# Kernel tuning notes

Measured on AMD Instinct MI355X. Metric: run time of the kernel, lower is better.

## Reference

```python
import jax, jax.numpy as jnp
import numpy as np

V, BLK, L, H, C, FF = 50257, 2048, 6, 8, 512, 2048
D = C // H  # head_dim = 64

def setup_inputs() -> dict:
    key = jax.random.key(0)
    ks = jax.random.split(key, 16)
    s = 0.02
    proj_std = 0.02 / np.sqrt(2 * L)
    return {
        'idx': jax.random.randint(ks[0], (2, 2048), 0, V, dtype=jnp.int64),
        'wte': jax.random.normal(ks[1], (V, C), jnp.float32) * s,
        'wpe': jax.random.normal(ks[2], (BLK, C), jnp.float32) * s,
        'ln1_w': jnp.ones((L, C), jnp.float32), 'ln1_b': jnp.zeros((L, C), jnp.float32),
        'c_attn_w': jax.random.normal(ks[3], (L, 3 * C, C), jnp.float32) * s,
        'c_proj_w': jax.random.normal(ks[4], (L, C, C), jnp.float32) * proj_std,
        'ln2_w': jnp.ones((L, C), jnp.float32), 'ln2_b': jnp.zeros((L, C), jnp.float32),
        'fc_w': jax.random.normal(ks[5], (L, FF, C), jnp.float32) * s,
        'proj_w': jax.random.normal(ks[6], (L, C, FF), jnp.float32) * proj_std,
        'lnf_w': jnp.ones((C,), jnp.float32), 'lnf_b': jnp.zeros((C,), jnp.float32),
    }

def _layernorm(x, w, b, eps=1e-5):
    mu = jnp.mean(x, axis=-1, keepdims=True)
    var = jnp.var(x, axis=-1, keepdims=True)
    return (x - mu) * jax.lax.rsqrt(var + eps) * w + b

def _attn(x, attn_w, proj_w, mask):
    B, T, _ = x.shape
    qkv = jnp.einsum('btc,fc->btf', x, attn_w)  # (B,T,3C)
    q, k, v = jnp.split(qkv, 3, axis=-1)
    q = q.reshape(B, T, H, D)
    k = k.reshape(B, T, H, D)
    v = v.reshape(B, T, H, D)
    scale = 1.0 / np.sqrt(D)
    att = jnp.einsum('bthd,bshd->bhts', q, k) * scale  # (B,H,T,T)
    att = jnp.where(mask, att, -jnp.inf)
    att = jax.nn.softmax(att, axis=-1)
    y = jnp.einsum('bhts,bshd->bthd', att, v).reshape(B, T, C)
    return jnp.einsum('btc,oc->bto', y, proj_w)

def reference(idx, wte, wpe, ln1_w, ln1_b, c_attn_w, c_proj_w, ln2_w, ln2_b, fc_w, proj_w, lnf_w, lnf_b):
    B, T = idx.shape
    pos = jnp.arange(T)
    x = wte[idx] + wpe[pos]  # (B,T,C); dropout p=0
    mask = jnp.tril(jnp.ones((T, T), bool))[None, None]
    for i in range(L):
        x = x + _attn(_layernorm(x, ln1_w[i], ln1_b[i]), c_attn_w[i], c_proj_w[i], mask)
        h = _layernorm(x, ln2_w[i], ln2_b[i])
        h = jax.nn.gelu(jnp.einsum('btc,fc->btf', h, fc_w[i]), approximate=False)
        x = x + jnp.einsum('btf,cf->btc', h, proj_w[i])
    x = _layernorm(x, lnf_w, lnf_b)
    logits = jnp.einsum('btc,vc->btv', x, wte)  # tied lm_head
    return logits
```

## Files before the change

kernel.cpp:

```cpp
#include <hip/hip_runtime.h>

typedef unsigned short u16;
typedef short bf16x8 __attribute__((ext_vector_type(8)));
typedef float f32x4 __attribute__((ext_vector_type(4)));
typedef unsigned short u16x4 __attribute__((ext_vector_type(4)));
typedef unsigned short u16x8 __attribute__((ext_vector_type(8)));
typedef unsigned int u32x2 __attribute__((ext_vector_type(2)));

#define B_ 2
#define T_ 2048
#define C_ 512
#define H_ 8
#define FF_ 2048
#define L_ 6
#define V_ 50257
#define M_ (B_*T_)

__device__ __forceinline__ u16 f2b(float f) {
  union { float f; unsigned u; } v; v.f = f;
  unsigned r = v.u + 0x7FFFu + ((v.u >> 16) & 1u);
  return (u16)(r >> 16);
}
__device__ __forceinline__ float b2f(u16 u) {
  union { unsigned u; float f; } v; v.u = ((unsigned)u) << 16; return v.f;
}
__device__ __forceinline__ unsigned pk_bf16(float lo, float hi) {
  unsigned r;
  asm volatile("v_cvt_pk_bf16_f32 %0, %1, %2" : "=v"(r) : "v"(lo), "v"(hi));
  return r;
}
__device__ __forceinline__ float exp2_fast(float x) {
  float r; asm("v_exp_f32 %0, %1" : "=v"(r) : "v"(x)); return r;
}
__device__ __forceinline__ float rcp_fast(float x) {
  float r; asm("v_rcp_f32 %0, %1" : "=v"(r) : "v"(x)); return r;
}

__device__ __forceinline__ void async16(const void* g, void* l) {
  __builtin_amdgcn_global_load_lds((const __attribute__((address_space(1))) unsigned int*)g,
                                   (__attribute__((address_space(3))) unsigned int*)l, 16, 0, 0);
}

template<int N> __device__ __forceinline__ void vwait() {
  if constexpr (N == 0) asm volatile("s_waitcnt vmcnt(0)" ::: "memory");
  else if constexpr (N == 2) asm volatile("s_waitcnt vmcnt(2)" ::: "memory");
  else if constexpr (N == 3) asm volatile("s_waitcnt vmcnt(3)" ::: "memory");
  else if constexpr (N == 4) asm volatile("s_waitcnt vmcnt(4)" ::: "memory");
}

__device__ __forceinline__ bf16x8 scale8(u16x8 v, float s) {
  union { bf16x8 b; unsigned u[4]; } r;
#pragma unroll
  for (int i = 0; i < 4; i++)
    r.u[i] = pk_bf16(b2f(v[2*i]) * s, b2f(v[2*i+1]) * s);
  return r.b;
}

__device__ __forceinline__ float gelu_f(float f) {
  float u = f * f;
  float inner = f * (0.7978845608028654f + 0.03567740814183056f * u);
  inner = fminf(fmaxf(inner, -15.f), 15.f);
  float a = exp2_fast(2.8853900817779268f * inner);
  return f * a * rcp_fast(a + 1.0f);
}

struct CvtArgs { const f32x4* s[5]; u16x4* d[5]; };
__global__ void cvt_all_k(CvtArgs a) {
  const int sizes[5] = { V_*C_/4, L_*3*C_*C_/4, L_*C_*C_/4, L_*FF_*C_/4, L_*C_*FF_/4 };
  int gid = blockIdx.x * blockDim.x + threadIdx.x;
  int stride = gridDim.x * blockDim.x;
#pragma unroll
  for (int seg = 0; seg < 5; seg++) {
    const f32x4* src = a.s[seg];
    u16x4* dst = a.d[seg];
    for (int i = gid; i < sizes[seg]; i += stride) {
      f32x4 v = src[i];
      u16x4 o;
      o[0] = f2b(v[0]); o[1] = f2b(v[1]); o[2] = f2b(v[2]); o[3] = f2b(v[3]);
      dst[i] = o;
    }
  }
}

__global__ void embed_k(const int* __restrict__ idx, const float* __restrict__ wte,
                        const float* __restrict__ wpe, float* __restrict__ x) {
  int t = blockIdx.x * 256 + threadIdx.x;
  int row = t >> 7;
  int c4 = t & 127;
  int tok = idx[row];
  int pos = row & (T_ - 1);
  f32x4 a = ((const f32x4*)(wte + (long)tok * C_))[c4];
  f32x4 p = ((const f32x4*)(wpe + (long)pos * C_))[c4];
  ((f32x4*)x)[t] = a + p;
}

__global__ void ln_k(const float* __restrict__ x, const float* __restrict__ w,
                     const float* __restrict__ b, u16* __restrict__ out) {
  int wv = threadIdx.x >> 6;
  int lane = threadIdx.x & 63;
  int row = blockIdx.x * 4 + wv;
  const f32x4* xr = (const f32x4*)(x + (long)row * C_);
  f32x4 v0 = xr[lane * 2], v1 = xr[lane * 2 + 1];
  float s = 0.f, s2 = 0.f;
#pragma unroll
  for (int j = 0; j < 4; j++) { s += v0[j] + v1[j]; s2 += v0[j]*v0[j] + v1[j]*v1[j]; }
#pragma unroll
  for (int off = 32; off >= 1; off >>= 1) { s += __shfl_xor(s, off); s2 += __shfl_xor(s2, off); }
  float mu = s * (1.f / C_);
  float inv = rsqrtf(s2 * (1.f / C_) - mu * mu + 1e-5f);
  const f32x4* wr = (const f32x4*)w;
  const f32x4* br = (const f32x4*)b;
  f32x4 w0 = wr[lane*2], w1 = wr[lane*2+1], b0 = br[lane*2], b1 = br[lane*2+1];
  u16x8 o;
#pragma unroll
  for (int j = 0; j < 4; j++) {
    o[j]     = f2b((v0[j] - mu) * inv * w0[j] + b0[j]);
    o[j + 4] = f2b((v1[j] - mu) * inv * w1[j] + b1[j]);
  }
  *(u16x8*)(out + (long)row * C_ + lane * 8) = o;
}

template<int EPI, int BM, int BN>
__global__ __launch_bounds__(256) void gemm_bt_k(
    const u16* __restrict__ A, const u16* __restrict__ Bw,
    u16* __restrict__ Cb, float* __restrict__ Cf,
    int N, int K, int ldc)
{
  constexpr int MT = BM / 32;
  constexpr int NT = BN / 32;
  constexpr int AJ = BM / 64;
  constexpr int BJ = BN / 64;
  constexpr int LPT = AJ + BJ;
  constexpr int MX = (M_ / BM) / 8;
  __shared__ __align__(16) u16 sA[3][BM * 32];
  __shared__ __align__(16) u16 sB[3][BN * 32];
  const int bid = blockIdx.x;
  const int xc = bid & 7;
  const int jj = bid >> 3;
  const int m0 = (xc * MX + (jj % MX)) * BM;
  const int n0 = (jj / MX) * BN;
  const int tid = threadIdx.x;
  const int w = tid >> 6;
  const int lane = tid & 63;
  const int wm = (w >> 1) * (BM / 2);
  const int wn = (w & 1) * (BN / 2);
  const int g = lane >> 4;
  const int l15 = lane & 15;
  const int sw3 = l15 & 3;

  f32x4 acc[MT][NT] = {};

  const int nk = K >> 5;
  const int ksw = ((tid & 3) ^ ((tid >> 2) & 3)) * 8;
  const u16* gA[AJ];
  const u16* gB[BJ];
#pragma unroll
  for (int j = 0; j < AJ; j++)
    gA[j] = A + (long)(m0 + (tid >> 2) + j * 64) * K + ksw;
#pragma unroll
  for (int j = 0; j < BJ; j++)
    gB[j] = Bw + (long)(n0 + (tid >> 2) + j * 64) * K + ksw;

  auto stage = [&](int buf, int kt) {
    int ko = kt << 5;
#pragma unroll
    for (int j = 0; j < AJ; j++)
      async16(gA[j] + ko, &sA[buf][(j * 256 + w * 64) * 8]);
#pragma unroll
    for (int j = 0; j < BJ; j++)
      async16(gB[j] + ko, &sB[buf][(j * 256 + w * 64) * 8]);
  };

  stage(0, 0);
  stage(1, 1);
  int cur = 0, nxt = 2;
  for (int kt = 0; kt < nk; kt++) {
    if (kt + 1 < nk) vwait<LPT>(); else vwait<0>();
    __builtin_amdgcn_s_barrier();
    if (kt + 2 < nk) stage(nxt, kt + 2);
    const u16* pa = sA[cur];
    const u16* pb = sB[cur];
    bf16x8 af[MT], bfr[NT];
#pragma unroll
    for (int mt = 0; mt < MT; mt++)
      af[mt] = *(const bf16x8*)(pa + (wm + mt * 16 + l15) * 32 + ((g ^ sw3) * 8));
#pragma unroll
    for (int nt = 0; nt < NT; nt++)
      bfr[nt] = *(const bf16x8*)(pb + (wn + nt * 16 + l15) * 32 + ((g ^ sw3) * 8));
#pragma unroll
    for (int mt = 0; mt < MT; mt++)
#pragma unroll
      for (int nt = 0; nt < NT; nt++)
        acc[mt][nt] = __builtin_amdgcn_mfma_f32_16x16x32_bf16(af[mt], bfr[nt], acc[mt][nt], 0, 0, 0);
    cur = (cur == 2) ? 0 : cur + 1;
    nxt = (nxt == 2) ? 0 : nxt + 1;
  }

#pragma unroll
  for (int mt = 0; mt < MT; mt++) {
    int m = m0 + wm + mt * 16 + g * 4;
#pragma unroll
    for (int nt = 0; nt < NT; nt++) {
      int n = n0 + wn + nt * 16 + l15;
      f32x4 v = acc[mt][nt];
#pragma unroll
      for (int r = 0; r < 4; r++) {
        long ci = (long)(m + r) * ldc + n;
        if (EPI == 0) {
          Cb[ci] = f2b(v[r]);
        } else {
          Cb[ci] = f2b(gelu_f(v[r]));
        }
      }
    }
  }
}

__global__ __launch_bounds__(256) void gemm_bt64_k(
    const u16* __restrict__ A, const u16* __restrict__ Bw,
    float* __restrict__ Cf, int N, int K, int ldc)
{
  __shared__ __align__(16) u16 sA[3][64 * 64];
  __shared__ __align__(16) u16 sB[3][64 * 64];
  const int bid = blockIdx.x;
  const int xc = bid & 7;
  const int jj = bid >> 3;
  const int m0 = (xc * 8 + (jj & 7)) * 64;
  const int n0 = (jj >> 3) * 64;
  const int tid = threadIdx.x;
  const int w = tid >> 6;
  const int lane = tid & 63;
  const int wm = (w >> 1) * 32;
  const int wn = (w & 1) * 32;
  const int g = lane >> 4;
  const int l15 = lane & 15;
  const int sw3 = l15 & 3;

  f32x4 acc[2][2] = {};

  const int nk = K >> 6;
  const int srow = tid >> 3;
  const int sl = tid & 7;
  const int kcol = (((sl & 4) | ((sl & 3) ^ (srow & 3)))) * 8;
  const u16* gA[2];
  const u16* gB[2];
#pragma unroll
  for (int j = 0; j < 2; j++) {
    gA[j] = A + (long)(m0 + srow + j * 32) * K + kcol;
    gB[j] = Bw + (long)(n0 + srow + j * 32) * K + kcol;
  }

  auto stage = [&](int buf, int kt) {
    int ko = kt << 6;
#pragma unroll
    for (int j = 0; j < 2; j++)
      async16(gA[j] + ko, &sA[buf][(j * 256 + w * 64) * 8]);
#pragma unroll
    for (int j = 0; j < 2; j++)
      async16(gB[j] + ko, &sB[buf][(j * 256 + w * 64) * 8]);
  };

  stage(0, 0);
  stage(1, 1);
  int cur = 0, nxt = 2;
  for (int kt = 0; kt < nk; kt++) {
    if (kt + 1 < nk) vwait<4>(); else vwait<0>();
    __builtin_amdgcn_s_barrier();
    if (kt + 2 < nk) stage(nxt, kt + 2);
    const u16* pa = sA[cur];
    const u16* pb = sB[cur];
#pragma unroll
    for (int h = 0; h < 2; h++) {
      bf16x8 af[2], bfr[2];
#pragma unroll
      for (int mt = 0; mt < 2; mt++)
        af[mt] = *(const bf16x8*)(pa + (wm + mt * 16 + l15) * 64 + (((g ^ sw3) + h * 4) * 8));
#pragma unroll
      for (int nt = 0; nt < 2; nt++)
        bfr[nt] = *(const bf16x8*)(pb + (wn + nt * 16 + l15) * 64 + (((g ^ sw3) + h * 4) * 8));
#pragma unroll
      for (int mt = 0; mt < 2; mt++)
#pragma unroll
        for (int nt = 0; nt < 2; nt++)
          acc[mt][nt] = __builtin_amdgcn_mfma_f32_16x16x32_bf16(af[mt], bfr[nt], acc[mt][nt], 0, 0, 0);
    }
    cur = (cur == 2) ? 0 : cur + 1;
    nxt = (nxt == 2) ? 0 : nxt + 1;
  }

#pragma unroll
  for (int mt = 0; mt < 2; mt++) {
    int m = m0 + wm + mt * 16 + g * 4;
#pragma unroll
    for (int nt = 0; nt < 2; nt++) {
      int n = n0 + wn + nt * 16 + l15;
      f32x4 v = acc[mt][nt];
#pragma unroll
      for (int r = 0; r < 4; r++)
        Cf[(long)(m + r) * ldc + n] += v[r];
    }
  }
}

__global__ __launch_bounds__(256) void gemm_lmhead_k(
    const u16* __restrict__ A, const u16* __restrict__ Bw,
    float* __restrict__ Cf, int N)
{
  constexpr int LPT = 4;
  __shared__ __align__(16) u16 sA[3][128 * 32];
  __shared__ __align__(16) u16 sB[3][128 * 32];
  const int K = 512;
  const int bid = blockIdx.x;
  const int xc = bid & 7;
  const int j = bid >> 3;
  const int mloc = j & 3;
  const int nidx = j >> 2;
  const int m0 = (xc * 4 + mloc) * 128;
  const int n0 = nidx * 128;
  const int tid = threadIdx.x;
  const int w = tid >> 6;
  const int lane = tid & 63;
  const int wm = (w >> 1) * 64;
  const int wn = (w & 1) * 64;
  const int g = lane >> 4;
  const int l15 = lane & 15;
  const int sw3 = l15 & 3;

  f32x4 acc[4][4] = {};

  const int ksw = ((tid & 3) ^ ((tid >> 2) & 3)) * 8;
  const u16* gA[2];
  const u16* gB[2];
#pragma unroll
  for (int jj = 0; jj < 2; jj++) {
    gA[jj] = A + (long)(m0 + (tid >> 2) + jj * 64) * K + ksw;
    int brow = n0 + (tid >> 2) + jj * 64; if (brow > N - 1) brow = N - 1;
    gB[jj] = Bw + (long)brow * K + ksw;
  }

  auto stage = [&](int buf, int kt) {
    int ko = kt << 5;
#pragma unroll
    for (int jj = 0; jj < 2; jj++)
      async16(gA[jj] + ko, &sA[buf][(jj * 256 + w * 64) * 8]);
#pragma unroll
    for (int jj = 0; jj < 2; jj++)
      async16(gB[jj] + ko, &sB[buf][(jj * 256 + w * 64) * 8]);
  };

  stage(0, 0);
  stage(1, 1);
  int cur = 0, nxt = 2;
  const int nk = K >> 5;
  for (int kt = 0; kt < nk; kt++) {
    if (kt + 1 < nk) vwait<LPT>(); else vwait<0>();
    __builtin_amdgcn_s_barrier();
    if (kt + 2 < nk) stage(nxt, kt + 2);
    const u16* pa = sA[cur];
    const u16* pb = sB[cur];
    bf16x8 af[4], bfr[4];
#pragma unroll
    for (int mt = 0; mt < 4; mt++)
      af[mt] = *(const bf16x8*)(pa + (wm + mt * 16 + l15) * 32 + ((g ^ sw3) * 8));
#pragma unroll
    for (int nt = 0; nt < 4; nt++)
      bfr[nt] = *(const bf16x8*)(pb + (wn + nt * 16 + l15) * 32 + ((g ^ sw3) * 8));
    __builtin_amdgcn_s_setprio(1);
#pragma unroll
    for (int mt = 0; mt < 4; mt++)
#pragma unroll
      for (int nt = 0; nt < 4; nt++)
        acc[mt][nt] = __builtin_amdgcn_mfma_f32_16x16x32_bf16(af[mt], bfr[nt], acc[mt][nt], 0, 0, 0);
    __builtin_amdgcn_s_setprio(0);
    cur = (cur == 2) ? 0 : cur + 1;
    nxt = (nxt == 2) ? 0 : nxt + 1;
  }

#pragma unroll
  for (int mt = 0; mt < 4; mt++) {
    int m = m0 + wm + mt * 16 + g * 4;
#pragma unroll
    for (int nt = 0; nt < 4; nt++) {
      int n = n0 + wn + nt * 16 + l15;
      f32x4 v = acc[mt][nt];
      if (n < N) {
#pragma unroll
        for (int r = 0; r < 4; r++)
          Cf[(long)(m + r) * N + n] = v[r];
      }
    }
  }
}

__global__ __launch_bounds__(256) void attn_k(const u16* __restrict__ qkv, u16* __restrict__ out) {
  const int bh = blockIdx.y;
  const int b = bh >> 3;
  const int h = bh & 7;
  const int tid = threadIdx.x;
  const int wv = tid >> 6;
  const int lane = tid & 63;
  const int g = lane >> 4;
  const int l15 = lane & 15;
  const int qblk = 31 - blockIdx.x;

  __shared__ __align__(16) u16 Ks[2][64 * 64];
  __shared__ __align__(16) u16 Vt[2][64 * 72];
  __shared__ __align__(16) u16 Ps[4][16 * 64];

  const long base = (long)b * T_ * 1536;
  const u16* kbase = qkv + base + 512 + h * 64;
  const u16* vbase = qkv + base + 1024 + h * 64;
  const int kq = tid & 15;
  const int dg = (tid >> 4) & 7;
  const float qscale = 0.18033688011112042f;

  const int q0 = qblk * 64 + wv * 16;

  const u16* qrow = qkv + base + (long)(q0 + l15) * 1536 + h * 64;
  bf16x8 qf0 = scale8(*(const u16x8*)(qrow + g * 8), qscale);
  bf16x8 qf1 = scale8(*(const u16x8*)(qrow + 32 + g * 8), qscale);

  f32x4 o[4] = {};
  float mrun[4] = {-1e30f, -1e30f, -1e30f, -1e30f};
  float lrun[4] = {0.f, 0.f, 0.f, 0.f};
  const int kvend = qblk * 64 + 64;

  u16x8 vreg[4];
#pragma unroll
  for (int i = 0; i < 2; i++) {
    int chunk = i * 256 + tid;
    int row = chunk >> 3, c8 = chunk & 7;
    async16(kbase + (long)row * 1536 + (c8 ^ (row & 7)) * 8,
            &Ks[0][(i * 256 + wv * 64) * 8]);
  }
  if (tid < 128) {
#pragma unroll
    for (int t = 0; t < 4; t++)
      vreg[t] = *(const u16x8*)(vbase + (long)(kq + 16 * t) * 1536 + dg * 8);
#pragma unroll
    for (int e = 0; e < 8; e++) {
      int d = dg * 8 + e;
      u32x2 wq = { (unsigned)vreg[0][e] | ((unsigned)vreg[1][e] << 16),
                   (unsigned)vreg[2][e] | ((unsigned)vreg[3][e] << 16) };
      *(u32x2*)(&Vt[0][d * 72 + kq * 4]) = wq;
    }
  }
  __syncthreads();

  int cur = 0;
  for (int j0 = 0; j0 < kvend; j0 += 64, cur ^= 1) {
    const bool more = (j0 + 64) < kvend;
    if (more) {
      int jn = j0 + 64;
#pragma unroll
      for (int i = 0; i < 2; i++) {
        int chunk = i * 256 + tid;
        int row = chunk >> 3, c8 = chunk & 7;
        async16(kbase + (long)(jn + row) * 1536 + (c8 ^ (row & 7)) * 8,
                &Ks[cur ^ 1][(i * 256 + wv * 64) * 8]);
      }
      if (tid < 128) {
#pragma unroll
        for (int t = 0; t < 4; t++)
          vreg[t] = *(const u16x8*)(vbase + (long)(jn + kq + 16 * t) * 1536 + dg * 8);
      }
    }

    f32x4 s[4] = {};
    const u16* kp = Ks[cur];
#pragma unroll
    for (int t = 0; t < 4; t++) {
      int row = t * 16 + l15;
      const u16* kr = kp + row * 64;
      bf16x8 k0 = *(const bf16x8*)(kr + ((g ^ (row & 7)) * 8));
      bf16x8 k1 = *(const bf16x8*)(kr + (((4 + g) ^ (row & 7)) * 8));
      s[t] = __builtin_amdgcn_mfma_f32_16x16x32_bf16(qf0, k0, s[t], 0, 0, 0);
      s[t] = __builtin_amdgcn_mfma_f32_16x16x32_bf16(qf1, k1, s[t], 0, 0, 0);
    }

    const bool diag = (j0 + 64) == kvend;
    u16* pw = Ps[wv];
#pragma unroll
    for (int r = 0; r < 4; r++) {
      int row = q0 + g * 4 + r;
      float v0 = s[0][r], v1 = s[1][r], v2 = s[2][r], v3 = s[3][r];
      if (diag) {
        if (j0 +      l15 > row) v0 = -1e30f;
        if (j0 + 16 + l15 > row) v1 = -1e30f;
        if (j0 + 32 + l15 > row) v2 = -1e30f;
        if (j0 + 48 + l15 > row) v3 = -1e30f;
      }
      float mloc = fmaxf(fmaxf(v0, v1), fmaxf(v2, v3));
      float m = mrun[r];
      if (!__all(mloc <= m + 8.0f)) {
        float mx = mloc;
        mx = fmaxf(mx, __shfl_xor(mx, 1));
        mx = fmaxf(mx, __shfl_xor(mx, 2));
        mx = fmaxf(mx, __shfl_xor(mx, 4));
        mx = fmaxf(mx, __shfl_xor(mx, 8));
        float mn = fmaxf(m, mx);
        float sc2 = exp2_fast(m - mn);
        lrun[r] *= sc2;
#pragma unroll
        for (int dt = 0; dt < 4; dt++) o[dt][r] *= sc2;
        m = mn; mrun[r] = mn;
      }
      float e0 = exp2_fast(v0 - m), e1 = exp2_fast(v1 - m);
      float e2 = exp2_fast(v2 - m), e3 = exp2_fast(v3 - m);
      lrun[r] += (e0 + e1) + (e2 + e3);
      u32x2 pkq = { pk_bf16(e0, e1), pk_bf16(e2, e3) };
      int prow = g * 4 + r;
      int byt = prow * 128 + ((((l15 >> 1) ^ (prow & 7)) << 4)) + (l15 & 1) * 8;
      *(u32x2*)((char*)pw + byt) = pkq;
    }

    const u16* vt = Vt[cur];
    bf16x8 pf0 = *(const bf16x8*)((char*)pw + l15 * 128 + (((g) ^ (l15 & 7)) << 4));
    bf16x8 pf1 = *(const bf16x8*)((char*)pw + l15 * 128 + (((4 + g) ^ (l15 & 7)) << 4));
#pragma unroll
    for (int dt = 0; dt < 4; dt++) {
      int d = dt * 16 + l15;
      bf16x8 vf0 = *(const bf16x8*)(vt + d * 72 + g * 8);
      bf16x8 vf1 = *(const bf16x8*)(vt + d * 72 + 32 + g * 8);
      o[dt] = __builtin_amdgcn_mfma_f32_16x16x32_bf16(pf0, vf0, o[dt], 0, 0, 0);
      o[dt] = __builtin_amdgcn_mfma_f32_16x16x32_bf16(pf1, vf1, o[dt], 0, 0, 0);
    }

    if (more && tid < 128) {
#pragma unroll
      for (int e = 0; e < 8; e++) {
        int d = dg * 8 + e;
        u32x2 wq = { (unsigned)vreg[0][e] | ((unsigned)vreg[1][e] << 16),
                     (unsigned)vreg[2][e] | ((unsigned)vreg[3][e] << 16) };
        *(u32x2*)(&Vt[cur ^ 1][d * 72 + kq * 4]) = wq;
      }
    }
    __syncthreads();
  }

#pragma unroll
  for (int r = 0; r < 4; r++) {
    float ls = lrun[r];
    ls += __shfl_xor(ls, 1); ls += __shfl_xor(ls, 2);
    ls += __shfl_xor(ls, 4); ls += __shfl_xor(ls, 8);
    float inv = 1.0f / ls;
    int row = q0 + g * 4 + r;
    u16* orow = out + (long)(b * T_ + row) * C_ + h * 64;
#pragma unroll
    for (int dt = 0; dt < 4; dt++)
      orow[dt * 16 + l15] = f2b(o[dt][r] * inv);
  }
}

extern "C" void kernel_launch(void* const* d_in, const int* in_sizes, int n_in,
                              void* d_out, int out_size, void* d_ws, size_t ws_size,
                              hipStream_t stream) {
  const int*   idx    = (const int*)  d_in[0];
  const float* wte    = (const float*)d_in[1];
  const float* wpe    = (const float*)d_in[2];
  const float* ln1w   = (const float*)d_in[3];
  const float* ln1b   = (const float*)d_in[4];
  const float* wattn  = (const float*)d_in[5];
  const float* wcproj = (const float*)d_in[6];
  const float* ln2w   = (const float*)d_in[7];
  const float* ln2b   = (const float*)d_in[8];
  const float* wfc    = (const float*)d_in[9];
  const float* wproj2 = (const float*)d_in[10];
  const float* lnfw   = (const float*)d_in[11];
  const float* lnfb   = (const float*)d_in[12];
  float* out = (float*)d_out;

  char* p = (char*)d_ws;
  size_t off = 0;
  auto alloc = [&](size_t bytes) -> void* {
    void* r = p + off; off += (bytes + 255) & ~(size_t)255; return r;
  };
  float* x    = (float*)alloc((size_t)M_ * C_ * 4);
  u16* xn     = (u16*)alloc((size_t)M_ * C_ * 2);
  u16* qkvb   = (u16*)alloc((size_t)M_ * 3 * C_ * 2);
  u16* attb   = (u16*)alloc((size_t)M_ * C_ * 2);
  u16* hb     = (u16*)alloc((size_t)M_ * FF_ * 2);
  u16* wteB   = (u16*)alloc((size_t)V_ * C_ * 2);
  u16* wattnB = (u16*)alloc((size_t)L_ * 3 * C_ * C_ * 2);
  u16* wprojB = (u16*)alloc((size_t)L_ * C_ * C_ * 2);
  u16* wfcB   = (u16*)alloc((size_t)L_ * FF_ * C_ * 2);
  u16* wp2B   = (u16*)alloc((size_t)L_ * C_ * FF_ * 2);
  if (off > ws_size) return;

  CvtArgs ca;
  ca.s[0] = (const f32x4*)wte;    ca.d[0] = (u16x4*)wteB;
  ca.s[1] = (const f32x4*)wattn;  ca.d[1] = (u16x4*)wattnB;
  ca.s[2] = (const f32x4*)wcproj; ca.d[2] = (u16x4*)wprojB;
  ca.s[3] = (const f32x4*)wfc;    ca.d[3] = (u16x4*)wfcB;
  ca.s[4] = (const f32x4*)wproj2; ca.d[4] = (u16x4*)wp2B;
  cvt_all_k<<<dim3(2048), dim3(256), 0, stream>>>(ca);

  embed_k<<<dim3(M_ * C_ / 4 / 256), dim3(256), 0, stream>>>(idx, wte, wpe, x);

  for (int l = 0; l < L_; l++) {
    ln_k<<<dim3(M_ / 4), dim3(256), 0, stream>>>(x, ln1w + l * C_, ln1b + l * C_, xn);
    gemm_bt_k<0, 64, 128><<<dim3(768), dim3(256), 0, stream>>>(
        xn, wattnB + (size_t)l * 3 * C_ * C_, qkvb, nullptr, 3 * C_, C_, 3 * C_);
    attn_k<<<dim3(32, B_ * H_), dim3(256), 0, stream>>>(qkvb, attb);
    gemm_bt64_k<<<dim3(512), dim3(256), 0, stream>>>(
        attb, wprojB + (size_t)l * C_ * C_, x, C_, C_, C_);
    ln_k<<<dim3(M_ / 4), dim3(256), 0, stream>>>(x, ln2w + l * C_, ln2b + l * C_, xn);
    gemm_bt_k<2, 128, 128><<<dim3(512), dim3(256), 0, stream>>>(
        xn, wfcB + (size_t)l * FF_ * C_, hb, nullptr, FF_, C_, FF_);
    gemm_bt64_k<<<dim3(512), dim3(256), 0, stream>>>(
        hb, wp2B + (size_t)l * C_ * FF_, x, C_, FF_, C_);
  }
  ln_k<<<dim3(M_ / 4), dim3(256), 0, stream>>>(x, lnfw, lnfb, xn);
  gemm_lmhead_k<<<dim3(8 * 1572), dim3(256), 0, stream>>>(xn, wteB, out, V_);
}
```

Baseline: 1.219 ms.

## Process three N-tiles per LM-head block with continuous K pipeline across tiles

The LM-head GEMM kernel now makes each block compute three consecutive 128-wide N tiles. It runs one continuous 48-step async-copy pipeline, and the accumulators are written out and zeroed after every 16 K-steps. The grid shrinks by a factor of three. This is meant to cut pipeline prologue and drain costs and block launch overhead, and to overlap one tile's epilogue stores with the next tile's loads. The trade-off is less parallelism, fewer blocks to spread across CUs, and a store phase inside the main loop. The 1572 N tiles split evenly into 524 groups, and out-of-range rows are clamped as before.

New measurement: 1.447 ms. +18.7%, slower.

```diff
diff --git a/kernel.cpp b/kernel.cpp
--- a/kernel.cpp
+++ b/kernel.cpp
@@ -306,7 +306,6 @@
     const u16* __restrict__ A, const u16* __restrict__ Bw,
     float* __restrict__ Cf, int N)
 {
-  constexpr int LPT = 4;
   __shared__ __align__(16) u16 sA[3][128 * 32];
   __shared__ __align__(16) u16 sB[3][128 * 32];
   const int K = 512;
@@ -314,9 +313,9 @@
   const int xc = bid & 7;
   const int j = bid >> 3;
   const int mloc = j & 3;
-  const int nidx = j >> 2;
+  const int ngrp = j >> 2;
   const int m0 = (xc * 4 + mloc) * 128;
-  const int n0 = nidx * 128;
+  const int nbase = ngrp * 3 * 128;
   const int tid = threadIdx.x;
   const int w = tid >> 6;
   const int lane = tid & 63;
@@ -330,32 +329,37 @@
 
   const int ksw = ((tid & 3) ^ ((tid >> 2) & 3)) * 8;
   const u16* gA[2];
-  const u16* gB[2];
+  const u16* gB[3][2];
 #pragma unroll
   for (int jj = 0; jj < 2; jj++) {
     gA[jj] = A + (long)(m0 + (tid >> 2) + jj * 64) * K + ksw;
-    int brow = n0 + (tid >> 2) + jj * 64; if (brow > N - 1) brow = N - 1;
-    gB[jj] = Bw + (long)brow * K + ksw;
-  }
-
-  auto stage = [&](int buf, int kt) {
-    int ko = kt << 5;
+#pragma unroll
+    for (int t = 0; t < 3; t++) {
+      int brow = nbase + t * 128 + (tid >> 2) + jj * 64;
+      if (brow > N - 1) brow = N - 1;
+      gB[t][jj] = Bw + (long)brow * K + ksw;
+    }
+  }
+
+  auto stage = [&](int buf, int ii) {
+    int ko = (ii & 15) << 5;
+    int t = ii >> 4;
 #pragma unroll
     for (int jj = 0; jj < 2; jj++)
       async16(gA[jj] + ko, &sA[buf][(jj * 256 + w * 64) * 8]);
 #pragma unroll
     for (int jj = 0; jj < 2; jj++)
-      async16(gB[jj] + ko, &sB[buf][(jj * 256 + w * 64) * 8]);
+      async16(gB[t][jj] + ko, &sB[buf][(jj * 256 + w * 64) * 8]);
   };
 
   stage(0, 0);
   stage(1, 1);
   int cur = 0, nxt = 2;
-  const int nk = K >> 5;
-  for (int kt = 0; kt < nk; kt++) {
-    if (kt + 1 < nk) vwait<LPT>(); else vwait<0>();
+  const int NI = 48;
+  for (int ii = 0; ii < NI; ii++) {
+    if (ii + 1 < NI) vwait<4>(); else vwait<0>();
     __builtin_amdgcn_s_barrier();
-    if (kt + 2 < nk) stage(nxt, kt + 2);
+    if (ii + 2 < NI) stage(nxt, ii + 2);
     const u16* pa = sA[cur];
     const u16* pb = sB[cur];
     bf16x8 af[4], bfr[4];
@@ -372,23 +376,26 @@
       for (int nt = 0; nt < 4; nt++)
         acc[mt][nt] = __builtin_amdgcn_mfma_f32_16x16x32_bf16(af[mt], bfr[nt], acc[mt][nt], 0, 0, 0);
     __builtin_amdgcn_s_setprio(0);
+    if ((ii & 15) == 15) {
+      int n0t = nbase + (ii >> 4) * 128;
+#pragma unroll
+      for (int mt = 0; mt < 4; mt++) {
+        int m = m0 + wm + mt * 16 + g * 4;
+#pragma unroll
+        for (int nt = 0; nt < 4; nt++) {
+          int n = n0t + wn + nt * 16 + l15;
+          f32x4 v = acc[mt][nt];
+          if (n < N) {
+#pragma unroll
+            for (int r = 0; r < 4; r++)
+              Cf[(long)(m + r) * N + n] = v[r];
+          }
+          acc[mt][nt] = f32x4{0.f, 0.f, 0.f, 0.f};
+        }
+      }
+    }
     cur = (cur == 2) ? 0 : cur + 1;
     nxt = (nxt == 2) ? 0 : nxt + 1;
-  }
-
-#pragma unroll
-  for (int mt = 0; mt < 4; mt++) {
-    int m = m0 + wm + mt * 16 + g * 4;
-#pragma unroll
-    for (int nt = 0; nt < 4; nt++) {
-      int n = n0 + wn + nt * 16 + l15;
-      f32x4 v = acc[mt][nt];
-      if (n < N) {
-#pragma unroll
-        for (int r = 0; r < 4; r++)
-          Cf[(long)(m + r) * N + n] = v[r];
-      }
-    }
   }
 }
 
@@ -611,5 +618,5 @@
         hb, wp2B + (size_t)l * C_ * FF_, x, C_, FF_, C_);
   }
   ln_k<<<dim3(M_ / 4), dim3(256), 0, stream>>>(x, lnfw, lnfb, xn);
-  gemm_lmhead_k<<<dim3(8 * 1572), dim3(256), 0, stream>>>(xn, wteB, out, V_);
-}
+  gemm_lmhead_k<<<dim3(8 * 524), dim3(256), 0, stream>>>(xn, wteB, out, V_);
+}
```

## Load lm_head GEMM operands directly from global memory, dropping LDS staging

Applied to the files above, without the earlier changes.

The lm_head GEMM kernel no longer stages A and B tiles through a triple-buffered shared-memory pipeline with async copies and barriers. Each wave now loads its MFMA fragments straight from global memory in a fully unrolled K loop and relies on L1/L2 caching for reuse across waves. This removes LDS traffic, barriers and wait overhead, and frees shared memory for higher occupancy. The cost is redundant global/cache loads, since two waves share each A and B row set, and less latency hiding.

Result: slower. 1.565 ms (+28.4%).

```diff
diff --git a/kernel.cpp b/kernel.cpp
--- a/kernel.cpp
+++ b/kernel.cpp
@@ -306,9 +306,6 @@
     const u16* __restrict__ A, const u16* __restrict__ Bw,
     float* __restrict__ Cf, int N)
 {
-  constexpr int LPT = 4;
-  __shared__ __align__(16) u16 sA[3][128 * 32];
-  __shared__ __align__(16) u16 sB[3][128 * 32];
   const int K = 512;
   const int bid = blockIdx.x;
   const int xc = bid & 7;
@@ -324,56 +321,36 @@
   const int wn = (w & 1) * 64;
   const int g = lane >> 4;
   const int l15 = lane & 15;
-  const int sw3 = l15 & 3;
 
   f32x4 acc[4][4] = {};
 
-  const int ksw = ((tid & 3) ^ ((tid >> 2) & 3)) * 8;
-  const u16* gA[2];
-  const u16* gB[2];
-#pragma unroll
-  for (int jj = 0; jj < 2; jj++) {
-    gA[jj] = A + (long)(m0 + (tid >> 2) + jj * 64) * K + ksw;
-    int brow = n0 + (tid >> 2) + jj * 64; if (brow > N - 1) brow = N - 1;
-    gB[jj] = Bw + (long)brow * K + ksw;
-  }
-
-  auto stage = [&](int buf, int kt) {
-    int ko = kt << 5;
-#pragma unroll
-    for (int jj = 0; jj < 2; jj++)
-      async16(gA[jj] + ko, &sA[buf][(jj * 256 + w * 64) * 8]);
-#pragma unroll
-    for (int jj = 0; jj < 2; jj++)
-      async16(gB[jj] + ko, &sB[buf][(jj * 256 + w * 64) * 8]);
-  };
-
-  stage(0, 0);
-  stage(1, 1);
-  int cur = 0, nxt = 2;
-  const int nk = K >> 5;
-  for (int kt = 0; kt < nk; kt++) {
-    if (kt + 1 < nk) vwait<LPT>(); else vwait<0>();
-    __builtin_amdgcn_s_barrier();
-    if (kt + 2 < nk) stage(nxt, kt + 2);
-    const u16* pa = sA[cur];
-    const u16* pb = sB[cur];
+  const u16* pa[4];
+  const u16* pb[4];
+#pragma unroll
+  for (int mt = 0; mt < 4; mt++)
+    pa[mt] = A + (long)(m0 + wm + mt * 16 + l15) * K + g * 8;
+#pragma unroll
+  for (int nt = 0; nt < 4; nt++) {
+    int brow = n0 + wn + nt * 16 + l15;
+    if (brow > N - 1) brow = N - 1;
+    pb[nt] = Bw + (long)brow * K + g * 8;
+  }
+
+#pragma unroll
+  for (int kt = 0; kt < 16; kt++) {
+    const int ko = kt * 32;
     bf16x8 af[4], bfr[4];
 #pragma unroll
     for (int mt = 0; mt < 4; mt++)
-      af[mt] = *(const bf16x8*)(pa + (wm + mt * 16 + l15) * 32 + ((g ^ sw3) * 8));
+      af[mt] = *(const bf16x8*)(pa[mt] + ko);
 #pragma unroll
     for (int nt = 0; nt < 4; nt++)
-      bfr[nt] = *(const bf16x8*)(pb + (wn + nt * 16 + l15) * 32 + ((g ^ sw3) * 8));
-    __builtin_amdgcn_s_setprio(1);
+      bfr[nt] = *(const bf16x8*)(pb[nt] + ko);
 #pragma unroll
     for (int mt = 0; mt < 4; mt++)
 #pragma unroll
       for (int nt = 0; nt < 4; nt++)
         acc[mt][nt] = __builtin_amdgcn_mfma_f32_16x16x32_bf16(af[mt], bfr[nt], acc[mt][nt], 0, 0, 0);
-    __builtin_amdgcn_s_setprio(0);
-    cur = (cur == 2) ? 0 : cur + 1;
-    nxt = (nxt == 2) ? 0 : nxt + 1;
   }
 
 #pragma unroll
```
